# Kernel optimization log

Hardware: AMD Instinct MI355X
Metric: run time of the kernel (lower is better)

The kernel has to match this reference:

```python
import jax, jax.numpy as jnp
import numpy as np

B, D = 4096, 1024

def setup_inputs() -> dict:
    key = jax.random.key(0)
    k1, k2, k3 = jax.random.split(key, 3)
    # q, p are row-stochastic probability distributions (original calls q.log())
    q = jax.nn.softmax(jax.random.normal(k1, (B, D), dtype=jnp.float32), axis=-1)
    p = jax.nn.softmax(jax.random.normal(k2, (B, D), dtype=jnp.float32), axis=-1)
    # binary same-class indicator matrix
    labels_matrix = jax.random.randint(k3, (B, B), 0, 2).astype(jnp.float32)
    return {"q": q, "p": p, "labels_matrix": labels_matrix}

def reference(q, p, labels_matrix):
    d = q.shape[1]
    log_q = jnp.log(q)
    log_p = jnp.log(p)
    # torch kl_div(log_q, p) = p * (log p - log q); mean over feature dim -> [B]
    kl_div = jnp.mean(p * (log_p - log_q), axis=1)
    # pairwise kl_dis[i, j] = mean_d p[j,d] * (log p[j,d] - log q[i,d])
    # = (sum_d p[j] log p[j] - (log_q @ p^T)[i, j]) / D  -- single GEMM, no BxBxD tensor
    p_entropy_term = jnp.sum(p * log_p, axis=1)          # [B]
    cross = log_q @ p.T                                   # [B, B]
    kl_dis = (p_entropy_term[None, :] - cross) / d        # [B, B]
    # original detaches kl_dis via .cpu().numpy()
    kl_dis = jax.lax.stop_gradient(kl_dis)
    positive = kl_div + jnp.sum(kl_dis * labels_matrix, axis=1)
    negative = jnp.sum(kl_dis * (1.0 - labels_matrix), axis=1)
    return jnp.sum(positive / negative)
```

## Files before the change

### kernel.cpp

```cpp
#include <hip/hip_runtime.h>
#include <hip/hip_bf16.h>
#include <stdint.h>

#define BROWS 4096
#define DDIM  1024

typedef __bf16 bf16_t;
typedef __bf16 bf16x8 __attribute__((ext_vector_type(8)));
typedef float  f32x4  __attribute__((ext_vector_type(4)));

#define LDS_STRIDE 68
#define GEMM_BLOCKS 512


__device__ __forceinline__ unsigned short f2bf_bits(float f) {
    union { float f; unsigned int u; } v; v.f = f;
    unsigned int u = v.u;
    unsigned int r = (u + 0x7fffu + ((u >> 16) & 1u)) >> 16;
    return (unsigned short)r;
}

__global__ __launch_bounds__(256) void prep_kernel(
    const float* __restrict__ q, const float* __restrict__ p,
    const float* __restrict__ L,
    bf16_t* __restrict__ lqb, bf16_t* __restrict__ pb,
    uint64_t* __restrict__ Lb,
    float* __restrict__ e, float* __restrict__ kld,
    float* __restrict__ CS, float* __restrict__ CL, float* __restrict__ EL,
    int* __restrict__ done)
{
    const int row = blockIdx.x;
    const int t   = threadIdx.x;
    const int wv  = t >> 6, ln = t & 63;

    const float4* q4 = (const float4*)(q + (size_t)row * DDIM);
    const float4* p4 = (const float4*)(p + (size_t)row * DDIM);
    float4 qv = q4[t];
    float4 pv = p4[t];

    float lq0 = __logf(qv.x), lq1 = __logf(qv.y), lq2 = __logf(qv.z), lq3 = __logf(qv.w);
    float lp0 = __logf(pv.x), lp1 = __logf(pv.y), lp2 = __logf(pv.z), lp3 = __logf(pv.w);

    float esum = pv.x * lp0 + pv.y * lp1 + pv.z * lp2 + pv.w * lp3;
    float ksum = pv.x * (lp0 - lq0) + pv.y * (lp1 - lq1)
               + pv.z * (lp2 - lq2) + pv.w * (lp3 - lq3);

    ushort4 uq, up;
    uq.x = f2bf_bits(lq0); uq.y = f2bf_bits(lq1); uq.z = f2bf_bits(lq2); uq.w = f2bf_bits(lq3);
    up.x = f2bf_bits(pv.x); up.y = f2bf_bits(pv.y); up.z = f2bf_bits(pv.z); up.w = f2bf_bits(pv.w);
    ((ushort4*)(lqb + (size_t)row * DDIM))[t] = uq;
    ((ushort4*)(pb  + (size_t)row * DDIM))[t] = up;

    const float4* L4 = (const float4*)(L + (size_t)row * BROWS);
    #pragma unroll
    for (int s = 0; s < 4; s++) {
        float4 lv = L4[s * 256 + t];
        unsigned long long b0 = __ballot(lv.x != 0.0f);
        unsigned long long b1 = __ballot(lv.y != 0.0f);
        unsigned long long b2 = __ballot(lv.z != 0.0f);
        unsigned long long b3 = __ballot(lv.w != 0.0f);
        if (ln < 4) {
            unsigned long long w = (ln == 0) ? b0 : (ln == 1) ? b1 : (ln == 2) ? b2 : b3;
            Lb[(size_t)row * 64 + (s * 4 + wv) * 4 + ln] = w;
        }
    }

    if (t == 0) { CS[row] = 0.f; CL[row] = 0.f; EL[row] = 0.f; }
    if (row == 0 && t == 0) *done = 0;

    #pragma unroll
    for (int off = 32; off > 0; off >>= 1) {
        esum += __shfl_down(esum, off);
        ksum += __shfl_down(ksum, off);
    }
    __shared__ float se[4], sk[4];
    if (ln == 0) { se[wv] = esum; sk[wv] = ksum; }
    __syncthreads();
    if (t == 0) {
        e[row]   = se[0] + se[1] + se[2] + se[3];
        kld[row] = (sk[0] + sk[1] + sk[2] + sk[3]) * (1.0f / DDIM);
    }
}

__global__ __launch_bounds__(512, 4) void gemm_epi_kernel(
    const bf16_t* __restrict__ Abf,
    const bf16_t* __restrict__ Bbf,
    const uint64_t* __restrict__ Lb,
    const float*  __restrict__ e,
    const float*  __restrict__ kld,
    float* __restrict__ CS, float* __restrict__ CL, float* __restrict__ EL,
    int* __restrict__ done, float* __restrict__ out)
{
    __shared__ __align__(16) bf16_t As[256 * LDS_STRIDE];
    __shared__ __align__(16) bf16_t Bs[128 * LDS_STRIDE];

    const int t    = threadIdx.x;
    const int b     = blockIdx.x;
    const int xcd   = b & 7;
    const int s     = b >> 3;
    const int i_idx = (xcd >> 2) * 8 + (s >> 3);
    const int j_idx = (xcd & 3) * 8 + (s & 7);
    const int i0   = i_idx * 256;
    const int j0   = j_idx * 128;
    const int wave = t >> 6;
    const int lane = t & 63;
    const int q4   = lane >> 4;
    const int ln   = lane & 15;
    const int wrow = wave & 3;
    const int wcol = wave >> 2;

    f32x4 acc[4][4];
    #pragma unroll
    for (int a = 0; a < 4; a++)
        #pragma unroll
        for (int bq = 0; bq < 4; bq++)
            acc[a][bq] = (f32x4){0.f, 0.f, 0.f, 0.f};

    const bf16_t* gAp[4]; int lA[4];
    const bf16_t* gBp[2]; int lB[2];
    #pragma unroll
    for (int n = 0; n < 4; n++) {
        const int id = t + n * 512;
        gAp[n] = Abf + (size_t)(i0 + (id >> 3)) * DDIM + (id & 7) * 8;
        lA[n]  = (id >> 3) * LDS_STRIDE + (id & 7) * 8;
    }
    #pragma unroll
    for (int n = 0; n < 2; n++) {
        const int id = t + n * 512;
        gBp[n] = Bbf + (size_t)(j0 + (id >> 3)) * DDIM + (id & 7) * 8;
        lB[n]  = (id >> 3) * LDS_STRIDE + (id & 7) * 8;
    }

    bf16x8 pfA[4], pfB[2];
    #pragma unroll
    for (int n = 0; n < 4; n++) pfA[n] = *(const bf16x8*)(gAp[n]);
    #pragma unroll
    for (int n = 0; n < 2; n++) pfB[n] = *(const bf16x8*)(gBp[n]);

    #pragma unroll 1
    for (int c = 0; c < DDIM / 64; ++c) {
        __syncthreads();
        #pragma unroll
        for (int n = 0; n < 4; n++) *(bf16x8*)(As + lA[n]) = pfA[n];
        #pragma unroll
        for (int n = 0; n < 2; n++) *(bf16x8*)(Bs + lB[n]) = pfB[n];
        __syncthreads();

        if (c + 1 < DDIM / 64) {
            const int k = (c + 1) * 64;
            #pragma unroll
            for (int n = 0; n < 4; n++) pfA[n] = *(const bf16x8*)(gAp[n] + k);
            #pragma unroll
            for (int n = 0; n < 2; n++) pfB[n] = *(const bf16x8*)(gBp[n] + k);
        }

        #pragma unroll
        for (int ks = 0; ks < 2; ks++) {
            bf16x8 af[4], bfr[4];
            #pragma unroll
            for (int mi = 0; mi < 4; mi++)
                af[mi] = *(const bf16x8*)(As + (wrow * 64 + mi * 16 + ln) * LDS_STRIDE
                                             + ks * 32 + q4 * 8);
            #pragma unroll
            for (int ni = 0; ni < 4; ni++)
                bfr[ni] = *(const bf16x8*)(Bs + (wcol * 64 + ni * 16 + ln) * LDS_STRIDE
                                              + ks * 32 + q4 * 8);
            #pragma unroll
            for (int mi = 0; mi < 4; mi++)
                #pragma unroll
                for (int ni = 0; ni < 4; ni++)
                    acc[mi][ni] = __builtin_amdgcn_mfma_f32_16x16x32_bf16(
                        af[mi], bfr[ni], acc[mi][ni], 0, 0, 0);
        }
    }

    const int i_base = i0 + wrow * 64;
    const int j_base = j0 + wcol * 64;
    const int wbase  = (j_base >> 8) * 4 + (ln & 3);
    const int bshift = ((j_base & 255) >> 2) + (ln >> 2);

    float e_j[4];
    #pragma unroll
    for (int ni = 0; ni < 4; ni++) e_j[ni] = e[j_base + ni * 16 + ln];

    #pragma unroll
    for (int mi = 0; mi < 4; mi++) {
        #pragma unroll
        for (int r = 0; r < 4; r++) {
            const int i = i_base + mi * 16 + q4 * 4 + r;
            const uint64_t m  = Lb[(size_t)i * 64 + wbase];
            const uint64_t ms = m >> bshift;
            float cs = 0.f, cl = 0.f, el = 0.f;
            #pragma unroll
            for (int ni = 0; ni < 4; ni++) {
                float c = acc[mi][ni][r];
                cs += c;
                if ((ms >> (ni * 4)) & 1ull) { cl += c; el += e_j[ni]; }
            }
            #pragma unroll
            for (int sft = 1; sft < 16; sft <<= 1) {
                cs += __shfl_xor(cs, sft);
                cl += __shfl_xor(cl, sft);
                el += __shfl_xor(el, sft);
            }
            if (ln == 0) {
                atomicAdd(&CS[i], cs);
                atomicAdd(&CL[i], cl);
                atomicAdd(&EL[i], el);
            }
        }
    }

    __asm__ volatile("s_waitcnt vmcnt(0)" ::: "memory");
    __syncthreads();
    __shared__ int sIsLast;
    if (t == 0) sIsLast = (atomicAdd(done, 1) == GEMM_BLOCKS - 1) ? 1 : 0;
    __syncthreads();
    if (sIsLast) {
        __shared__ float sred[8];
        __shared__ float sEtot;
        const int wv8 = t >> 6;

        float ssum = 0.f;
        #pragma unroll
        for (int j = t; j < BROWS; j += 512) ssum += e[j];
        #pragma unroll
        for (int off = 32; off > 0; off >>= 1) ssum += __shfl_down(ssum, off);
        if (lane == 0) sred[wv8] = ssum;
        __syncthreads();
        if (t == 0) {
            float a = 0.f;
            #pragma unroll
            for (int k = 0; k < 8; k++) a += sred[k];
            sEtot = a;
        }
        __syncthreads();
        const float Etot = sEtot;
        const float invD = 1.0f / DDIM;

        float rs = 0.f;
        #pragma unroll
        for (int i = t; i < BROWS; i += 512) {
            float el = __hip_atomic_load(&EL[i], __ATOMIC_RELAXED, __HIP_MEMORY_SCOPE_AGENT);
            float cl = __hip_atomic_load(&CL[i], __ATOMIC_RELAXED, __HIP_MEMORY_SCOPE_AGENT);
            float cs = __hip_atomic_load(&CS[i], __ATOMIC_RELAXED, __HIP_MEMORY_SCOPE_AGENT);
            float pos = kld[i] + (el - cl) * invD;
            float neg = (Etot - el - cs + cl) * invD;
            rs += pos / neg;
        }
        __syncthreads();
        #pragma unroll
        for (int off = 32; off > 0; off >>= 1) rs += __shfl_down(rs, off);
        if (lane == 0) sred[wv8] = rs;
        __syncthreads();
        if (t == 0) {
            float a = 0.f;
            #pragma unroll
            for (int k = 0; k < 8; k++) a += sred[k];
            out[0] = a;
        }
    }
}

extern "C" void kernel_launch(void* const* d_in, const int* in_sizes, int n_in,
                              void* d_out, int out_size, void* d_ws, size_t ws_size,
                              hipStream_t stream)
{
    const float* q = (const float*)d_in[0];
    const float* p = (const float*)d_in[1];
    const float* L = (const float*)d_in[2];
    float* out = (float*)d_out;

    char* ws = (char*)d_ws;
    bf16_t* lqb = (bf16_t*)ws;
    bf16_t* pb  = (bf16_t*)(ws + (size_t)BROWS * DDIM * 2);
    float*  e   = (float*)(ws + (size_t)BROWS * DDIM * 4);
    float*  kld = e + BROWS;
    float*  CS  = kld + BROWS;
    float*  CL  = CS + BROWS;
    float*  EL  = CL + BROWS;
    uint64_t* Lb = (uint64_t*)(EL + BROWS);
    int*    done = (int*)(Lb + (size_t)BROWS * 64);

    prep_kernel<<<BROWS, 256, 0, stream>>>(q, p, L, lqb, pb, Lb, e, kld, CS, CL, EL, done);

    gemm_epi_kernel<<<GEMM_BLOCKS, 512, 0, stream>>>(lqb, pb, Lb, e, kld,
                                                     CS, CL, EL, done, out);
}
```

Before: 175.2 us.

## Use direct global-to-LDS loads with XOR swizzle and 128x128 tiles

Replaces the register-prefetch plus padded-LDS staging with global_load_lds direct copies into an XOR-swizzled unpadded LDS layout. The GEMM tile shrinks from 256x128 with 512 threads to 128x128 with 256 threads, doubling the block count to 1024. This is meant to cut VGPR staging cost and LDS bank conflicts. In exchange it drops the software prefetch overlap: each k-step waits on vmcnt(0) before compute.

```diff
diff --git a/kernel.cpp b/kernel.cpp
--- a/kernel.cpp
+++ b/kernel.cpp
@@ -8,9 +8,9 @@
 typedef __bf16 bf16_t;
 typedef __bf16 bf16x8 __attribute__((ext_vector_type(8)));
 typedef float  f32x4  __attribute__((ext_vector_type(4)));
-
-#define LDS_STRIDE 68
-#define GEMM_BLOCKS 512
+typedef unsigned int u32;
+
+#define GEMM_BLOCKS 1024
 
 
 __device__ __forceinline__ unsigned short f2bf_bits(float f) {
@@ -18,6 +18,12 @@
     unsigned int u = v.u;
     unsigned int r = (u + 0x7fffu + ((u >> 16) & 1u)) >> 16;
     return (unsigned short)r;
+}
+
+__device__ __forceinline__ void gload16(const void* g, void* l) {
+    __builtin_amdgcn_global_load_lds(
+        (const __attribute__((address_space(1))) u32*)g,
+        (__attribute__((address_space(3))) u32*)l, 16, 0, 0);
 }
 
 __global__ __launch_bounds__(256) void prep_kernel(
@@ -82,7 +88,7 @@
     }
 }
 
-__global__ __launch_bounds__(512, 4) void gemm_epi_kernel(
+__global__ __launch_bounds__(256) void gemm_epi_kernel(
     const bf16_t* __restrict__ Abf,
     const bf16_t* __restrict__ Bbf,
     const uint64_t* __restrict__ Lb,
@@ -91,23 +97,23 @@
     float* __restrict__ CS, float* __restrict__ CL, float* __restrict__ EL,
     int* __restrict__ done, float* __restrict__ out)
 {
-    __shared__ __align__(16) bf16_t As[256 * LDS_STRIDE];
-    __shared__ __align__(16) bf16_t Bs[128 * LDS_STRIDE];
-
-    const int t    = threadIdx.x;
+    __shared__ __align__(16) bf16_t As[128 * 64];
+    __shared__ __align__(16) bf16_t Bs[128 * 64];
+
+    const int t     = threadIdx.x;
     const int b     = blockIdx.x;
     const int xcd   = b & 7;
     const int s     = b >> 3;
-    const int i_idx = (xcd >> 2) * 8 + (s >> 3);
+    const int i_idx = (xcd >> 2) * 16 + (s >> 3);
     const int j_idx = (xcd & 3) * 8 + (s & 7);
-    const int i0   = i_idx * 256;
-    const int j0   = j_idx * 128;
-    const int wave = t >> 6;
-    const int lane = t & 63;
-    const int q4   = lane >> 4;
-    const int ln   = lane & 15;
-    const int wrow = wave & 3;
-    const int wcol = wave >> 2;
+    const int i0    = i_idx * 128;
+    const int j0    = j_idx * 128;
+    const int wave  = t >> 6;
+    const int lane  = t & 63;
+    const int q4    = lane >> 4;
+    const int ln    = lane & 15;
+    const int wrow  = wave & 1;
+    const int wcol  = wave >> 1;
 
     f32x4 acc[4][4];
     #pragma unroll
@@ -116,55 +122,43 @@
         for (int bq = 0; bq < 4; bq++)
             acc[a][bq] = (f32x4){0.f, 0.f, 0.f, 0.f};
 
-    const bf16_t* gAp[4]; int lA[4];
-    const bf16_t* gBp[2]; int lB[2];
+    const bf16_t* gA[4]; const bf16_t* gB[4];
+    char* lA[4]; char* lB[4];
     #pragma unroll
     for (int n = 0; n < 4; n++) {
-        const int id = t + n * 512;
-        gAp[n] = Abf + (size_t)(i0 + (id >> 3)) * DDIM + (id & 7) * 8;
-        lA[n]  = (id >> 3) * LDS_STRIDE + (id & 7) * 8;
-    }
-    #pragma unroll
-    for (int n = 0; n < 2; n++) {
-        const int id = t + n * 512;
-        gBp[n] = Bbf + (size_t)(j0 + (id >> 3)) * DDIM + (id & 7) * 8;
-        lB[n]  = (id >> 3) * LDS_STRIDE + (id & 7) * 8;
-    }
-
-    bf16x8 pfA[4], pfB[2];
-    #pragma unroll
-    for (int n = 0; n < 4; n++) pfA[n] = *(const bf16x8*)(gAp[n]);
-    #pragma unroll
-    for (int n = 0; n < 2; n++) pfB[n] = *(const bf16x8*)(gBp[n]);
+        const int id   = t + n * 256;
+        const int row  = id >> 3;
+        const int gcol = ((id & 7) ^ (row & 7)) * 8;
+        gA[n] = Abf + (size_t)(i0 + row) * DDIM + gcol;
+        gB[n] = Bbf + (size_t)(j0 + row) * DDIM + gcol;
+        lA[n] = (char*)As + id * 16;
+        lB[n] = (char*)Bs + id * 16;
+    }
+
+    const int swz = (ln & 7) << 4;
 
     #pragma unroll 1
     for (int c = 0; c < DDIM / 64; ++c) {
         __syncthreads();
         #pragma unroll
-        for (int n = 0; n < 4; n++) *(bf16x8*)(As + lA[n]) = pfA[n];
-        #pragma unroll
-        for (int n = 0; n < 2; n++) *(bf16x8*)(Bs + lB[n]) = pfB[n];
-        __syncthreads();
-
-        if (c + 1 < DDIM / 64) {
-            const int k = (c + 1) * 64;
-            #pragma unroll
-            for (int n = 0; n < 4; n++) pfA[n] = *(const bf16x8*)(gAp[n] + k);
-            #pragma unroll
-            for (int n = 0; n < 2; n++) pfB[n] = *(const bf16x8*)(gBp[n] + k);
-        }
+        for (int n = 0; n < 4; n++) gload16(gA[n] + c * 64, lA[n]);
+        #pragma unroll
+        for (int n = 0; n < 4; n++) gload16(gB[n] + c * 64, lB[n]);
+        __asm__ volatile("s_waitcnt vmcnt(0)" ::: "memory");
+        __syncthreads();
 
         #pragma unroll
         for (int ks = 0; ks < 2; ks++) {
+            const int cb = (ks * 64 + q4 * 16) ^ swz;
             bf16x8 af[4], bfr[4];
             #pragma unroll
             for (int mi = 0; mi < 4; mi++)
-                af[mi] = *(const bf16x8*)(As + (wrow * 64 + mi * 16 + ln) * LDS_STRIDE
-                                             + ks * 32 + q4 * 8);
+                af[mi] = *(const bf16x8*)((const char*)As
+                           + (wrow * 64 + mi * 16 + ln) * 128 + cb);
             #pragma unroll
             for (int ni = 0; ni < 4; ni++)
-                bfr[ni] = *(const bf16x8*)(Bs + (wcol * 64 + ni * 16 + ln) * LDS_STRIDE
-                                              + ks * 32 + q4 * 8);
+                bfr[ni] = *(const bf16x8*)((const char*)Bs
+                           + (wcol * 64 + ni * 16 + ln) * 128 + cb);
             #pragma unroll
             for (int mi = 0; mi < 4; mi++)
                 #pragma unroll
@@ -193,9 +187,9 @@
             float cs = 0.f, cl = 0.f, el = 0.f;
             #pragma unroll
             for (int ni = 0; ni < 4; ni++) {
-                float c = acc[mi][ni][r];
-                cs += c;
-                if ((ms >> (ni * 4)) & 1ull) { cl += c; el += e_j[ni]; }
+                float cv = acc[mi][ni][r];
+                cs += cv;
+                if ((ms >> (ni * 4)) & 1ull) { cl += cv; el += e_j[ni]; }
             }
             #pragma unroll
             for (int sft = 1; sft < 16; sft <<= 1) {
@@ -217,21 +211,21 @@
     if (t == 0) sIsLast = (atomicAdd(done, 1) == GEMM_BLOCKS - 1) ? 1 : 0;
     __syncthreads();
     if (sIsLast) {
-        __shared__ float sred[8];
+        __shared__ float sred[4];
         __shared__ float sEtot;
-        const int wv8 = t >> 6;
+        const int wv = t >> 6;
 
         float ssum = 0.f;
         #pragma unroll
-        for (int j = t; j < BROWS; j += 512) ssum += e[j];
+        for (int j = t; j < BROWS; j += 256) ssum += e[j];
         #pragma unroll
         for (int off = 32; off > 0; off >>= 1) ssum += __shfl_down(ssum, off);
-        if (lane == 0) sred[wv8] = ssum;
+        if (lane == 0) sred[wv] = ssum;
         __syncthreads();
         if (t == 0) {
             float a = 0.f;
             #pragma unroll
-            for (int k = 0; k < 8; k++) a += sred[k];
+            for (int k = 0; k < 4; k++) a += sred[k];
             sEtot = a;
         }
         __syncthreads();
@@ -240,7 +234,7 @@
 
         float rs = 0.f;
         #pragma unroll
-        for (int i = t; i < BROWS; i += 512) {
+        for (int i = t; i < BROWS; i += 256) {
             float el = __hip_atomic_load(&EL[i], __ATOMIC_RELAXED, __HIP_MEMORY_SCOPE_AGENT);
             float cl = __hip_atomic_load(&CL[i], __ATOMIC_RELAXED, __HIP_MEMORY_SCOPE_AGENT);
             float cs = __hip_atomic_load(&CS[i], __ATOMIC_RELAXED, __HIP_MEMORY_SCOPE_AGENT);
@@ -251,12 +245,12 @@
         __syncthreads();
         #pragma unroll
         for (int off = 32; off > 0; off >>= 1) rs += __shfl_down(rs, off);
-        if (lane == 0) sred[wv8] = rs;
+        if (lane == 0) sred[wv] = rs;
         __syncthreads();
         if (t == 0) {
             float a = 0.f;
             #pragma unroll
-            for (int k = 0; k < 8; k++) a += sred[k];
+            for (int k = 0; k < 4; k++) a += sred[k];
             out[0] = a;
         }
     }
@@ -284,6 +278,6 @@
 
     prep_kernel<<<BROWS, 256, 0, stream>>>(q, p, L, lqb, pb, Lb, e, kld, CS, CL, EL, done);
 
-    gemm_epi_kernel<<<GEMM_BLOCKS, 512, 0, stream>>>(lqb, pb, Lb, e, kld,
+    gemm_epi_kernel<<<GEMM_BLOCKS, 256, 0, stream>>>(lqb, pb, Lb, e, kld,
                                                      CS, CL, EL, done, out);
 }
```

Result: slower. 196.9 us (+12.4%).

## Rewrite GEMM mainloop with 256x256 tiles and async global-to-LDS double buffering

Applied to the files above, without the earlier changes.

Enlarges the output tile from 256x128 to 256x256 per block, which halves the grid to 256 blocks and doubles the per-wave accumulator to 8x4 fragments. The register-staged global loads are replaced by direct global_load_lds transfers into a swizzled, double-buffered LDS layout. A phased schedule with s_waitcnt and explicit barriers overlaps loads with MFMA work, and s_setprio raises priority around the MFMAs. This is meant to cut global traffic per FLOP and hide load latency, at the cost of fewer blocks (256 for 256 CUs), lower occupancy and higher register pressure.

```diff
diff --git a/kernel.cpp b/kernel.cpp
--- a/kernel.cpp
+++ b/kernel.cpp
@@ -8,9 +8,11 @@
 typedef __bf16 bf16_t;
 typedef __bf16 bf16x8 __attribute__((ext_vector_type(8)));
 typedef float  f32x4  __attribute__((ext_vector_type(4)));
-
-#define LDS_STRIDE 68
-#define GEMM_BLOCKS 512
+typedef unsigned int u32;
+
+#define GEMM_BLOCKS 256
+#define NT  16
+#define NIT 8
 
 
 __device__ __forceinline__ unsigned short f2bf_bits(float f) {
@@ -18,6 +20,12 @@
     unsigned int u = v.u;
     unsigned int r = (u + 0x7fffu + ((u >> 16) & 1u)) >> 16;
     return (unsigned short)r;
+}
+
+__device__ __forceinline__ void gload16(const void* g, void* l) {
+    __builtin_amdgcn_global_load_lds(
+        (const __attribute__((address_space(1))) u32*)g,
+        (__attribute__((address_space(3))) u32*)l, 16, 0, 0);
 }
 
 __global__ __launch_bounds__(256) void prep_kernel(
@@ -82,7 +90,54 @@
     }
 }
 
-__global__ __launch_bounds__(512, 4) void gemm_epi_kernel(
+
+#define VM4 __asm__ volatile("s_waitcnt vmcnt(4)" ::: "memory")
+#define VM0 __asm__ volatile("s_waitcnt vmcnt(0)" ::: "memory")
+#define NOP ((void)0)
+
+#define STAGE_A(KT, KH) do { \
+    const int _ko = (KT) * 64 + (KH) * 32; \
+    char* _r = (char*)As + ((((KT) & 1) * 2 + (KH)) * 16384); \
+    gload16(gA0 + _ko, _r + dst0); \
+    gload16(gA1 + _ko, _r + dst1); \
+} while (0)
+
+#define STAGE_B(KT, KH) do { \
+    const int _ko = (KT) * 64 + (KH) * 32; \
+    char* _r = (char*)Bs + ((((KT) & 1) * 2 + (KH)) * 16384); \
+    gload16(gB0 + _ko, _r + dst0); \
+    gload16(gB1 + _ko, _r + dst1); \
+} while (0)
+
+#define PHASE(DB, KH, FMB, LOADB, STG, WAITS) do { \
+    const char* _Ar = (const char*)As + (((DB) * 2 + (KH)) * 16384); \
+    const char* _Br = (const char*)Bs + (((DB) * 2 + (KH)) * 16384); \
+    bf16x8 _af[4]; \
+    _Pragma("unroll") \
+    for (int _f = 0; _f < 4; ++_f) \
+        _af[_f] = *(const bf16x8*)(_Ar + aOff + ((FMB) + _f) * 1024); \
+    if (LOADB) { \
+        _Pragma("unroll") \
+        for (int _n = 0; _n < 4; ++_n) \
+            bfr[_n] = *(const bf16x8*)(_Br + bOff + _n * 1024); \
+    } \
+    STG; \
+    __asm__ volatile("" ::: "memory"); \
+    __builtin_amdgcn_s_barrier(); \
+    __builtin_amdgcn_s_setprio(1); \
+    _Pragma("unroll") \
+    for (int _f = 0; _f < 4; ++_f) \
+        _Pragma("unroll") \
+        for (int _n = 0; _n < 4; ++_n) \
+            acc[(FMB) + _f][_n] = __builtin_amdgcn_mfma_f32_16x16x32_bf16( \
+                _af[_f], bfr[_n], acc[(FMB) + _f][_n], 0, 0, 0); \
+    __builtin_amdgcn_s_setprio(0); \
+    WAITS; \
+    __asm__ volatile("" ::: "memory"); \
+    __builtin_amdgcn_s_barrier(); \
+} while (0)
+
+__global__ __launch_bounds__(512, 2) void gemm_epi_kernel(
     const bf16_t* __restrict__ Abf,
     const bf16_t* __restrict__ Bbf,
     const uint64_t* __restrict__ Lb,
@@ -91,111 +146,99 @@
     float* __restrict__ CS, float* __restrict__ CL, float* __restrict__ EL,
     int* __restrict__ done, float* __restrict__ out)
 {
-    __shared__ __align__(16) bf16_t As[256 * LDS_STRIDE];
-    __shared__ __align__(16) bf16_t Bs[128 * LDS_STRIDE];
+    __shared__ __align__(16) bf16_t As[2 * 2 * 256 * 32];
+    __shared__ __align__(16) bf16_t Bs[2 * 2 * 256 * 32];
 
     const int t    = threadIdx.x;
-    const int b     = blockIdx.x;
-    const int xcd   = b & 7;
-    const int s     = b >> 3;
-    const int i_idx = (xcd >> 2) * 8 + (s >> 3);
-    const int j_idx = (xcd & 3) * 8 + (s & 7);
+    const int b    = blockIdx.x;
+    const int xcd  = b & 7;
+    const int s    = b >> 3;
+    const int i_idx = (xcd >> 1) * 4 + (s >> 3);
+    const int j_idx = (xcd & 1) * 8 + (s & 7);
     const int i0   = i_idx * 256;
-    const int j0   = j_idx * 128;
+    const int j0   = j_idx * 256;
     const int wave = t >> 6;
     const int lane = t & 63;
-    const int q4   = lane >> 4;
+    const int q4u  = lane >> 4;
     const int ln   = lane & 15;
-    const int wrow = wave & 3;
-    const int wcol = wave >> 2;
-
-    f32x4 acc[4][4];
-    #pragma unroll
-    for (int a = 0; a < 4; a++)
-        #pragma unroll
-        for (int bq = 0; bq < 4; bq++)
-            acc[a][bq] = (f32x4){0.f, 0.f, 0.f, 0.f};
-
-    const bf16_t* gAp[4]; int lA[4];
-    const bf16_t* gBp[2]; int lB[2];
-    #pragma unroll
-    for (int n = 0; n < 4; n++) {
-        const int id = t + n * 512;
-        gAp[n] = Abf + (size_t)(i0 + (id >> 3)) * DDIM + (id & 7) * 8;
-        lA[n]  = (id >> 3) * LDS_STRIDE + (id & 7) * 8;
-    }
-    #pragma unroll
-    for (int n = 0; n < 2; n++) {
-        const int id = t + n * 512;
-        gBp[n] = Bbf + (size_t)(j0 + (id >> 3)) * DDIM + (id & 7) * 8;
-        lB[n]  = (id >> 3) * LDS_STRIDE + (id & 7) * 8;
-    }
-
-    bf16x8 pfA[4], pfB[2];
-    #pragma unroll
-    for (int n = 0; n < 4; n++) pfA[n] = *(const bf16x8*)(gAp[n]);
-    #pragma unroll
-    for (int n = 0; n < 2; n++) pfB[n] = *(const bf16x8*)(gBp[n]);
+    const int wm   = wave >> 2;
+    const int wn   = wave & 3;
+
+    const int aRow  = wm * 128 + ln;
+    const int aSlot = q4u ^ ((aRow >> 1) & 3);
+    const int aOff  = aRow * 64 + aSlot * 16;
+    const int bRow  = wn * 64 + ln;
+    const int bSlot = q4u ^ ((bRow >> 1) & 3);
+    const int bOff  = bRow * 64 + bSlot * 16;
+
+    const int id20 = t, id21 = t + 512;
+    const int row0 = id20 >> 2, row1 = id21 >> 2;
+    const int ss0  = (id20 & 3) ^ ((row0 >> 1) & 3);
+    const int ss1  = (id21 & 3) ^ ((row1 >> 1) & 3);
+    const bf16_t* gA0 = Abf + (size_t)(i0 + row0) * DDIM + ss0 * 8;
+    const bf16_t* gA1 = Abf + (size_t)(i0 + row1) * DDIM + ss1 * 8;
+    const bf16_t* gB0 = Bbf + (size_t)(j0 + row0) * DDIM + ss0 * 8;
+    const bf16_t* gB1 = Bbf + (size_t)(j0 + row1) * DDIM + ss1 * 8;
+    const int dst0 = id20 * 16, dst1 = id21 * 16;
+
+    f32x4 acc[8][4];
+    #pragma unroll
+    for (int a = 0; a < 8; a++)
+        #pragma unroll
+        for (int n = 0; n < 4; n++)
+            acc[a][n] = (f32x4){0.f, 0.f, 0.f, 0.f};
+    bf16x8 bfr[4];
+
+    STAGE_A(0, 0); STAGE_B(0, 0);
+    STAGE_A(0, 1); STAGE_B(0, 1);
+    STAGE_A(1, 0); STAGE_B(1, 0);
+    VM4;
+    __asm__ volatile("" ::: "memory");
+    __builtin_amdgcn_s_barrier();
 
     #pragma unroll 1
-    for (int c = 0; c < DDIM / 64; ++c) {
-        __syncthreads();
-        #pragma unroll
-        for (int n = 0; n < 4; n++) *(bf16x8*)(As + lA[n]) = pfA[n];
-        #pragma unroll
-        for (int n = 0; n < 2; n++) *(bf16x8*)(Bs + lB[n]) = pfB[n];
-        __syncthreads();
-
-        if (c + 1 < DDIM / 64) {
-            const int k = (c + 1) * 64;
-            #pragma unroll
-            for (int n = 0; n < 4; n++) pfA[n] = *(const bf16x8*)(gAp[n] + k);
-            #pragma unroll
-            for (int n = 0; n < 2; n++) pfB[n] = *(const bf16x8*)(gBp[n] + k);
-        }
-
-        #pragma unroll
-        for (int ks = 0; ks < 2; ks++) {
-            bf16x8 af[4], bfr[4];
-            #pragma unroll
-            for (int mi = 0; mi < 4; mi++)
-                af[mi] = *(const bf16x8*)(As + (wrow * 64 + mi * 16 + ln) * LDS_STRIDE
-                                             + ks * 32 + q4 * 8);
-            #pragma unroll
-            for (int ni = 0; ni < 4; ni++)
-                bfr[ni] = *(const bf16x8*)(Bs + (wcol * 64 + ni * 16 + ln) * LDS_STRIDE
-                                              + ks * 32 + q4 * 8);
-            #pragma unroll
-            for (int mi = 0; mi < 4; mi++)
-                #pragma unroll
-                for (int ni = 0; ni < 4; ni++)
-                    acc[mi][ni] = __builtin_amdgcn_mfma_f32_16x16x32_bf16(
-                        af[mi], bfr[ni], acc[mi][ni], 0, 0, 0);
-        }
-    }
-
-    const int i_base = i0 + wrow * 64;
-    const int j_base = j0 + wcol * 64;
+    for (int it = 0; it < NIT - 1; ++it) {
+        const int k1 = 2 * it + 1, k2 = 2 * it + 2, k3 = 2 * it + 3;
+        PHASE(0, 0, 0, true,  STAGE_A(k1, 1), NOP);
+        PHASE(0, 0, 4, false, STAGE_B(k1, 1), NOP);
+        PHASE(0, 1, 0, true,  STAGE_A(k2, 0), NOP);
+        PHASE(0, 1, 4, false, STAGE_B(k2, 0), VM4);
+        PHASE(1, 0, 0, true,  STAGE_A(k2, 1), NOP);
+        PHASE(1, 0, 4, false, STAGE_B(k2, 1), NOP);
+        PHASE(1, 1, 0, true,  STAGE_A(k3, 0), NOP);
+        PHASE(1, 1, 4, false, STAGE_B(k3, 0), VM4);
+    }
+    PHASE(0, 0, 0, true,  STAGE_A(15, 1), NOP);
+    PHASE(0, 0, 4, false, STAGE_B(15, 1), NOP);
+    PHASE(0, 1, 0, true,  NOP, NOP);
+    PHASE(0, 1, 4, false, NOP, VM0);
+    PHASE(1, 0, 0, true,  NOP, NOP);
+    PHASE(1, 0, 4, false, NOP, NOP);
+    PHASE(1, 1, 0, true,  NOP, NOP);
+    PHASE(1, 1, 4, false, NOP, NOP);
+
+    const int i_base = i0 + wm * 128;
+    const int j_base = j0 + wn * 64;
     const int wbase  = (j_base >> 8) * 4 + (ln & 3);
     const int bshift = ((j_base & 255) >> 2) + (ln >> 2);
 
     float e_j[4];
     #pragma unroll
-    for (int ni = 0; ni < 4; ni++) e_j[ni] = e[j_base + ni * 16 + ln];
-
-    #pragma unroll
-    for (int mi = 0; mi < 4; mi++) {
+    for (int fn = 0; fn < 4; fn++) e_j[fn] = e[j_base + fn * 16 + ln];
+
+    #pragma unroll
+    for (int fm = 0; fm < 8; fm++) {
         #pragma unroll
         for (int r = 0; r < 4; r++) {
-            const int i = i_base + mi * 16 + q4 * 4 + r;
+            const int i = i_base + fm * 16 + q4u * 4 + r;
             const uint64_t m  = Lb[(size_t)i * 64 + wbase];
             const uint64_t ms = m >> bshift;
             float cs = 0.f, cl = 0.f, el = 0.f;
             #pragma unroll
-            for (int ni = 0; ni < 4; ni++) {
-                float c = acc[mi][ni][r];
-                cs += c;
-                if ((ms >> (ni * 4)) & 1ull) { cl += c; el += e_j[ni]; }
+            for (int fn = 0; fn < 4; fn++) {
+                float cv = acc[fm][fn][r];
+                cs += cv;
+                if ((ms >> (fn * 4)) & 1ull) { cl += cv; el += e_j[fn]; }
             }
             #pragma unroll
             for (int sft = 1; sft < 16; sft <<= 1) {
```

After: 176.2 us. No clear change (+0.6%).
